# Kernel tuning notes

Measured on AMD Instinct MI355X. Metric: run time of the kernel, lower is better.

The kernel has to match this reference:

```python
import jax, jax.numpy as jnp
from jax import lax
import numpy as np

N_ITERS = 1000
LR = 0.1
EPS = 1e-8


def _log_mag_loss(sos, target_dB):
    """MSE between 20*log10(|sosfreqz(sos)|) and target_dB (matches LogMagTargetFrequencyLoss)."""
    n = target_dB.shape[-1]
    w = jnp.linspace(0.0, np.pi, n)            # [n] freqs in [0, pi]
    z1 = jnp.exp(-1j * w.astype(jnp.complex64))  # e^{-jw}, [n]
    z2 = z1 * z1                               # e^{-2jw}
    b = sos[:, :3].astype(jnp.complex64)       # [16,3] numerator coeffs
    a = sos[:, 3:].astype(jnp.complex64)       # [16,3] denominator coeffs
    # per-section response: (b0 + b1 z^-1 + b2 z^-2) / (a0 + a1 z^-1 + a2 z^-2), [16,n]
    B = b[:, 0:1] + b[:, 1:2] * z1[None, :] + b[:, 2:3] * z2[None, :]
    A = a[:, 0:1] + a[:, 1:2] * z1[None, :] + a[:, 2:3] * z2[None, :]
    H = jnp.prod(B / A, axis=0)                # cascade of sections, [n]
    mag = jnp.sqrt(jnp.real(H) ** 2 + jnp.imag(H) ** 2)
    input_dB = 20.0 * jnp.log10(mag + EPS)
    return jnp.mean((input_dB - target_dB) ** 2)


def setup_inputs() -> dict:
    key = jax.random.key(0)
    k1, k2 = jax.random.split(key)
    sos_init = jax.random.uniform(k1, (16, 6), dtype=jnp.float32)  # torch.rand(16,6)
    target_dB = jax.random.normal(k2, (512,), dtype=jnp.float32) * 6.0  # dB-scale target curve
    return {"sos_init": sos_init, "target_dB": target_dB}


def reference(sos_init, target_dB):
    grad_fn = jax.grad(_log_mag_loss)

    def step(sos, _):
        g = grad_fn(sos, target_dB)
        return sos - LR * g, None  # plain SGD step (no momentum)

    sos_final, _ = lax.scan(step, sos_init, None, length=N_ITERS)
    return sos_final
```

## Files before the change

kernel.cpp:

```cpp
#include <hip/hip_runtime.h>
#include <math.h>

#define TPB 1024

typedef float v2f __attribute__((ext_vector_type(2)));
typedef float v4f __attribute__((ext_vector_type(4)));

static __device__ __forceinline__ v2f mk2(float x, float y) {
    v2f r; r.x = x; r.y = y; return r;
}
static __device__ __forceinline__ v2f fma2(v2f a, v2f b, v2f c) {
    return __builtin_elementwise_fma(a, b, c);
}
static __device__ __forceinline__ v2f rcp2(v2f x) {
    v2f r;
    r.x = __builtin_amdgcn_rcpf(x.x);
    r.y = __builtin_amdgcn_rcpf(x.y);
    return r;
}

static __device__ __forceinline__ void quad_allsum2(float& a, float& b) {
    asm("s_nop 1\n\t"
        "v_add_f32 %0, %0, %0 quad_perm:[1,0,3,2] row_mask:0xf bank_mask:0xf bound_ctrl:0\n\t"
        "v_add_f32 %1, %1, %1 quad_perm:[1,0,3,2] row_mask:0xf bank_mask:0xf bound_ctrl:0\n\t"
        "s_nop 0\n\t"
        "v_add_f32 %0, %0, %0 quad_perm:[2,3,0,1] row_mask:0xf bank_mask:0xf bound_ctrl:0\n\t"
        "v_add_f32 %1, %1, %1 quad_perm:[2,3,0,1] row_mask:0xf bank_mask:0xf bound_ctrl:0"
        : "+v"(a), "+v"(b));
}

__device__ __forceinline__ void red6_s8(float i0, float i1, float i2,
                                        float i3, float i4, float i5,
                                        float& o0, float& o1, float& o2,
                                        float& o3, float& o4, float& o5) {
    asm("s_nop 1\n\t"
        "v_add_f32 %0, %6, %6  row_shr:8 row_mask:0xf bank_mask:0xf bound_ctrl:0\n\t"
        "v_add_f32 %3, %9, %9  row_shr:8 row_mask:0xf bank_mask:0xf bound_ctrl:0\n\t"
        "v_add_f32 %1, %7, %7  row_shr:8 row_mask:0xf bank_mask:0xf bound_ctrl:0\n\t"
        "v_add_f32 %4, %10, %10 row_shr:8 row_mask:0xf bank_mask:0xf bound_ctrl:0\n\t"
        "v_add_f32 %2, %8, %8  row_shr:8 row_mask:0xf bank_mask:0xf bound_ctrl:0\n\t"
        "v_add_f32 %5, %11, %11 row_shr:8 row_mask:0xf bank_mask:0xf bound_ctrl:0"
        : "=&v"(o0), "=&v"(o1), "=&v"(o2), "=&v"(o3), "=&v"(o4), "=&v"(o5)
        : "v"(i0), "v"(i1), "v"(i2), "v"(i3), "v"(i4), "v"(i5));
}

__device__ __forceinline__ void red4_g32(float& a, float& b,
                                         float& c, float& d) {
    asm("s_nop 1\n\t"
        "v_add_f32 %0, %0, %0 row_shr:1 row_mask:0xf bank_mask:0xf bound_ctrl:0\n\t"
        "v_add_f32 %1, %1, %1 row_shr:1 row_mask:0xf bank_mask:0xf bound_ctrl:0\n\t"
        "v_add_f32 %2, %2, %2 row_shr:1 row_mask:0xf bank_mask:0xf bound_ctrl:0\n\t"
        "v_add_f32 %3, %3, %3 row_shr:1 row_mask:0xf bank_mask:0xf bound_ctrl:0\n\t"
        "v_add_f32 %0, %0, %0 row_shr:2 row_mask:0xf bank_mask:0xf bound_ctrl:0\n\t"
        "v_add_f32 %1, %1, %1 row_shr:2 row_mask:0xf bank_mask:0xf bound_ctrl:0\n\t"
        "v_add_f32 %2, %2, %2 row_shr:2 row_mask:0xf bank_mask:0xf bound_ctrl:0\n\t"
        "v_add_f32 %3, %3, %3 row_shr:2 row_mask:0xf bank_mask:0xf bound_ctrl:0\n\t"
        "v_add_f32 %0, %0, %0 row_shr:4 row_mask:0xf bank_mask:0xf bound_ctrl:0\n\t"
        "v_add_f32 %1, %1, %1 row_shr:4 row_mask:0xf bank_mask:0xf bound_ctrl:0\n\t"
        "v_add_f32 %2, %2, %2 row_shr:4 row_mask:0xf bank_mask:0xf bound_ctrl:0\n\t"
        "v_add_f32 %3, %3, %3 row_shr:4 row_mask:0xf bank_mask:0xf bound_ctrl:0\n\t"
        "v_add_f32 %0, %0, %0 row_shr:8 row_mask:0xf bank_mask:0xf bound_ctrl:0\n\t"
        "v_add_f32 %1, %1, %1 row_shr:8 row_mask:0xf bank_mask:0xf bound_ctrl:0\n\t"
        "v_add_f32 %2, %2, %2 row_shr:8 row_mask:0xf bank_mask:0xf bound_ctrl:0\n\t"
        "v_add_f32 %3, %3, %3 row_shr:8 row_mask:0xf bank_mask:0xf bound_ctrl:0\n\t"
        "v_add_f32 %0, %0, %0 row_bcast:15 row_mask:0xa bank_mask:0xf\n\t"
        "v_add_f32 %1, %1, %1 row_bcast:15 row_mask:0xa bank_mask:0xf\n\t"
        "v_add_f32 %2, %2, %2 row_bcast:15 row_mask:0xa bank_mask:0xf\n\t"
        "v_add_f32 %3, %3, %3 row_bcast:15 row_mask:0xa bank_mask:0xf"
        : "+v"(a), "+v"(b), "+v"(c), "+v"(d));
}

__device__ __forceinline__ int cmap(int k) {
    return (k < 3) ? 2 * k : 2 * k - 5;
}

#define GPAD 132

__global__
__attribute__((amdgpu_flat_work_group_size(TPB, TPB), amdgpu_waves_per_eu(4, 4)))
void sgd_filter(const float* __restrict__ sos_in,
                const float* __restrict__ target,
                float* __restrict__ out) {
    __shared__ __align__(16) float sos[96];
    __shared__ __align__(16) float gpart[128][GPAD];

    const int tid = threadIdx.x;
    const int qd  = tid >> 2;
    const int pos = tid & 3;
    const float* secbase = &sos[pos * 24];

    if (tid < 96) sos[(tid / 6) * 6 + cmap(tid % 6)] = sos_in[tid];

    const int c    = tid >> 5;
    const int j    = tid & 31;
    const int slot = c >> 1;
    const int h    = c & 1;
    const int us   = 4 * (slot & 3) + (slot >> 2);
    const bool owner = ((tid & 31) == 31);
    const float* urp = &gpart[j][4 * c];
    float k0 = 0.f, k1 = 0.f, k2 = 0.f, k3 = 0.f;
    if (owner) {
        if (h == 0) {
            k0 = sos_in[6 * us + 0]; k1 = sos_in[6 * us + 3];
            k2 = sos_in[6 * us + 1]; k3 = sos_in[6 * us + 4];
        } else {
            k0 = sos_in[6 * us + 2]; k1 = sos_in[6 * us + 5];
        }
    }

    const double step = 3.14159265358979323846 / 511.0;
    const float w0 = (float)((double)(2 * qd) * step);
    const float w1 = (float)((double)(2 * qd + 1) * step);
    const float c10 = cosf(w0), s10 = -sinf(w0);
    const float c20 = c10 * c10 - s10 * s10, s20 = 2.0f * c10 * s10;
    const float c11 = cosf(w1), s11 = -sinf(w1);
    const float c21 = c11 * c11 - s11 * s11, s21 = 2.0f * c11 * s11;
    const float2 tg = *(const float2*)&target[2 * qd];
    const float KC = 40.0f / (512.0f * 2.302585092994046f);

    const v2f c1v0 = mk2(c10, c10), s1v0 = mk2(s10, s10);
    const v2f c2v0 = mk2(c20, c20), s2v0 = mk2(s20, s20);
    const v2f c1v1 = mk2(c11, c11), s1v1 = mk2(s11, s11);
    const v2f c2v1 = mk2(c21, c21), s2v1 = mk2(s21, s21);

    __syncthreads();

    v2f RA0, RA1, RA2, RA3, IA0, IA1, IA2, IA3;
    v2f RB0, RB1, RB2, RB3, IB0, IB1, IB2, IB3;
    v2f NA0, NA1, NA2, NA3, NB0, NB1, NB2, NB3;

#define SEC_EVAL(sl, BA0, BA1, BA2)                                         \
    {                                                                       \
        const v2f ba0 = BA0, ba1 = BA1, ba2 = BA2;                          \
        RA##sl = fma2(ba2, c2v0, fma2(ba1, c1v0, ba0));                     \
        IA##sl = fma2(ba2, s2v0, ba1 * s1v0);                               \
        NA##sl = fma2(RA##sl, RA##sl, IA##sl * IA##sl);                     \
        RB##sl = fma2(ba2, c2v1, fma2(ba1, c1v1, ba0));                     \
        IB##sl = fma2(ba2, s2v1, ba1 * s1v1);                               \
        NB##sl = fma2(RB##sl, RB##sl, IB##sl * IB##sl);                     \
    }

#define SEC_BWD(sl)                                                         \
    {                                                                       \
        const v2f PA = WA##sl * RA##sl;                                     \
        const v2f QA = WA##sl * IA##sl;                                     \
        const v2f PB = WB##sl * RB##sl;                                     \
        const v2f QB = WB##sl * IB##sl;                                     \
        const v2f P  = PA + PB;                                             \
        const v2f G1 = fma2(c1v1, PB, fma2(s1v1, QB,                        \
                       fma2(c1v0, PA, s1v0 * QA)));                         \
        const v2f G2 = fma2(c2v1, PB, fma2(s2v1, QB,                        \
                       fma2(c2v0, PA, s2v0 * QA)));                         \
        float g0, g1, g2, g3, g4, g5;                                       \
        red6_s8(P.x, G1.x, G2.x, P.y, G1.y, G2.y,                           \
                g0, g1, g2, g3, g4, g5);                                    \
        if ((tid & 15) >= 8) {                                              \
            float* p = &gpart[((tid >> 4) << 1) | ((tid >> 2) & 1)]         \
                             [8 * (4 * (sl) + pos)];                        \
            *(float4*)p       = make_float4(g0, g3, g1, g4);                \
            *(float2*)(p + 4) = make_float2(g2, g5);                        \
        }                                                                   \
    }

    for (int it = 0; it < 1000; ++it) {
        const float4 q0 = *(const float4*)(secbase + 0);
        const float4 q1 = *(const float4*)(secbase + 4);
        const float4 q2 = *(const float4*)(secbase + 8);
        const float4 q3 = *(const float4*)(secbase + 12);
        const float4 q4 = *(const float4*)(secbase + 16);
        const float4 q5 = *(const float4*)(secbase + 20);
        SEC_EVAL(0, mk2(q0.x, q0.y), mk2(q0.z, q0.w), mk2(q1.x, q1.y))
        SEC_EVAL(1, mk2(q1.z, q1.w), mk2(q2.x, q2.y), mk2(q2.z, q2.w))
        SEC_EVAL(2, mk2(q3.x, q3.y), mk2(q3.z, q3.w), mk2(q4.x, q4.y))
        SEC_EVAL(3, mk2(q4.z, q4.w), mk2(q5.x, q5.y), mk2(q5.z, q5.w))

        const v2f tA01 = NA0 * NA1, tA23 = NA2 * NA3;
        const v2f mA   = tA01 * tA23;
        const v2f iA   = rcp2(mA);
        const v2f tB01 = NB0 * NB1, tB23 = NB2 * NB3;
        const v2f mB   = tB01 * tB23;
        const v2f iB   = rcp2(mB);
        float L0 = __builtin_amdgcn_logf(mA.x * iA.y);
        float L1 = __builtin_amdgcn_logf(mB.x * iB.y);

        quad_allsum2(L0, L1);

        const float mag0   = __builtin_amdgcn_exp2f(0.5f * L0);
        const float magpe0 = mag0 + 1e-8f;
        const float indB0  = 6.020599913279624f * __builtin_amdgcn_logf(magpe0);
        const float K0 = KC * (indB0 - tg.x) * mag0 * __builtin_amdgcn_rcpf(magpe0);
        const float mag1   = __builtin_amdgcn_exp2f(0.5f * L1);
        const float magpe1 = mag1 + 1e-8f;
        const float indB1  = 6.020599913279624f * __builtin_amdgcn_logf(magpe1);
        const float K1 = KC * (indB1 - tg.y) * mag1 * __builtin_amdgcn_rcpf(magpe1);
        const v2f KK0 = mk2(K0, -K0);
        const v2f KK1 = mk2(K1, -K1);

        const v2f jA   = KK0 * iA;
        const v2f jA01 = jA * tA23, jA23 = jA * tA01;
        const v2f WA0 = jA01 * NA1, WA1 = jA01 * NA0;
        const v2f WA2 = jA23 * NA3, WA3 = jA23 * NA2;
        const v2f jB   = KK1 * iB;
        const v2f jB01 = jB * tB23, jB23 = jB * tB01;
        const v2f WB0 = jB01 * NB1, WB1 = jB01 * NB0;
        const v2f WB2 = jB23 * NB3, WB3 = jB23 * NB2;

        SEC_BWD(0) SEC_BWD(1) SEC_BWD(2) SEC_BWD(3)
        __syncthreads();

        {
            const v4f p0 = *(const v4f*)urp;
            const v4f p1 = *(const v4f*)(urp + 32 * GPAD);
            const v4f p2 = *(const v4f*)(urp + 64 * GPAD);
            const v4f p3 = *(const v4f*)(urp + 96 * GPAD);
            const v4f s = (p0 + p1) + (p2 + p3);
            float t0 = s.x, t1 = s.y, t2 = s.z, t3 = s.w;
            red4_g32(t0, t1, t2, t3);
            if (owner) {
                k0 = fmaf(-0.1f, t0, k0);
                k1 = fmaf(-0.1f, t1, k1);
                k2 = fmaf(-0.1f, t2, k2);
                k3 = fmaf(-0.1f, t3, k3);
                if (h == 0) {
                    *(float2*)&sos[6 * us]     = make_float2(k0, k1);
                    *(float2*)&sos[6 * us + 2] = make_float2(k2, k3);
                } else {
                    *(float2*)&sos[6 * us + 4] = make_float2(k0, k1);
                }
            }
        }
        __syncthreads();
    }

    if (owner) {
        if (h == 0) {
            out[6 * us + 0] = k0; out[6 * us + 3] = k1;
            out[6 * us + 1] = k2; out[6 * us + 4] = k3;
        } else {
            out[6 * us + 2] = k0; out[6 * us + 5] = k1;
        }
    }
}

extern "C" void kernel_launch(void* const* d_in, const int* in_sizes, int n_in,
                              void* d_out, int out_size, void* d_ws, size_t ws_size,
                              hipStream_t stream) {
    const float* sos_in = (const float*)d_in[0];
    const float* target = (const float*)d_in[1];
    float* outp = (float*)d_out;
    hipLaunchKernelGGL(sgd_filter, dim3(1), dim3(TPB), 0, stream, sos_in, target, outp);
}
```

Measured before the change: 1.960 ms.

## Pack gradient partials densely, replace log-sum with product-sqrt, fold dB constants

The gradient partial buffer is repacked so each writer lane stores 24 contiguous floats with six float4 stores, and GPAD shrinks to 100. Only 24 waves, with 4 coefficients each, now perform the reduction and the float4 sos update, replacing the earlier half-slot layout with its branching. The per-quad log-sum followed by exp2 is replaced with a DPP product reduction followed by sqrt, and the dB scaling constants are folded into one fma. The product form could overflow or underflow in float32 where the log-sum form would not.

```diff
diff --git a/kernel.cpp b/kernel.cpp
--- a/kernel.cpp
+++ b/kernel.cpp
@@ -19,13 +19,13 @@
     return r;
 }
 
-static __device__ __forceinline__ void quad_allsum2(float& a, float& b) {
+static __device__ __forceinline__ void quad_allprod2(float& a, float& b) {
     asm("s_nop 1\n\t"
-        "v_add_f32 %0, %0, %0 quad_perm:[1,0,3,2] row_mask:0xf bank_mask:0xf bound_ctrl:0\n\t"
-        "v_add_f32 %1, %1, %1 quad_perm:[1,0,3,2] row_mask:0xf bank_mask:0xf bound_ctrl:0\n\t"
+        "v_mul_f32 %0, %0, %0 quad_perm:[1,0,3,2] row_mask:0xf bank_mask:0xf bound_ctrl:0\n\t"
+        "v_mul_f32 %1, %1, %1 quad_perm:[1,0,3,2] row_mask:0xf bank_mask:0xf bound_ctrl:0\n\t"
         "s_nop 0\n\t"
-        "v_add_f32 %0, %0, %0 quad_perm:[2,3,0,1] row_mask:0xf bank_mask:0xf bound_ctrl:0\n\t"
-        "v_add_f32 %1, %1, %1 quad_perm:[2,3,0,1] row_mask:0xf bank_mask:0xf bound_ctrl:0"
+        "v_mul_f32 %0, %0, %0 quad_perm:[2,3,0,1] row_mask:0xf bank_mask:0xf bound_ctrl:0\n\t"
+        "v_mul_f32 %1, %1, %1 quad_perm:[2,3,0,1] row_mask:0xf bank_mask:0xf bound_ctrl:0"
         : "+v"(a), "+v"(b));
 }
 
@@ -73,8 +73,12 @@
 __device__ __forceinline__ int cmap(int k) {
     return (k < 3) ? 2 * k : 2 * k - 5;
 }
-
-#define GPAD 132
+__device__ __forceinline__ int oidx(int cid) {
+    const int s = cid / 6, p = cid % 6;
+    return 6 * s + ((p & 1) ? 3 + (p >> 1) : (p >> 1));
+}
+
+#define GPAD 100
 
 __global__
 __attribute__((amdgpu_flat_work_group_size(TPB, TPB), amdgpu_waves_per_eu(4, 4)))
@@ -88,24 +92,21 @@
     const int qd  = tid >> 2;
     const int pos = tid & 3;
     const float* secbase = &sos[pos * 24];
+    const int brow = ((tid >> 4) << 1) | ((tid >> 2) & 1);
 
     if (tid < 96) sos[(tid / 6) * 6 + cmap(tid % 6)] = sos_in[tid];
 
     const int c    = tid >> 5;
     const int j    = tid & 31;
-    const int slot = c >> 1;
-    const int h    = c & 1;
-    const int us   = 4 * (slot & 3) + (slot >> 2);
-    const bool owner = ((tid & 31) == 31);
-    const float* urp = &gpart[j][4 * c];
+    const bool upd   = (c < 24);
+    const bool owner = upd && (j == 31);
+    const float* urp = &gpart[j][4 * (c & 31)];
+    const int oi0 = oidx(4 * c + 0), oi1 = oidx(4 * c + 1);
+    const int oi2 = oidx(4 * c + 2), oi3 = oidx(4 * c + 3);
     float k0 = 0.f, k1 = 0.f, k2 = 0.f, k3 = 0.f;
     if (owner) {
-        if (h == 0) {
-            k0 = sos_in[6 * us + 0]; k1 = sos_in[6 * us + 3];
-            k2 = sos_in[6 * us + 1]; k3 = sos_in[6 * us + 4];
-        } else {
-            k0 = sos_in[6 * us + 2]; k1 = sos_in[6 * us + 5];
-        }
+        k0 = sos_in[oi0]; k1 = sos_in[oi1];
+        k2 = sos_in[oi2]; k3 = sos_in[oi3];
     }
 
     const double step = 3.14159265358979323846 / 511.0;
@@ -117,6 +118,9 @@
     const float c21 = c11 * c11 - s11 * s11, s21 = 2.0f * c11 * s11;
     const float2 tg = *(const float2*)&target[2 * qd];
     const float KC = 40.0f / (512.0f * 2.302585092994046f);
+    const float A2   = KC * 6.020599913279624f;
+    const float nKt0 = -KC * tg.x;
+    const float nKt1 = -KC * tg.y;
 
     const v2f c1v0 = mk2(c10, c10), s1v0 = mk2(s10, s10);
     const v2f c2v0 = mk2(c20, c20), s2v0 = mk2(s20, s20);
@@ -140,7 +144,8 @@
         NB##sl = fma2(RB##sl, RB##sl, IB##sl * IB##sl);                     \
     }
 
-#define SEC_BWD(sl)                                                         \
+#define SEC_BWD(sl, g)                                                      \
+    float g##0, g##1, g##2, g##3, g##4, g##5;                               \
     {                                                                       \
         const v2f PA = WA##sl * RA##sl;                                     \
         const v2f QA = WA##sl * IA##sl;                                     \
@@ -151,15 +156,8 @@
                        fma2(c1v0, PA, s1v0 * QA)));                         \
         const v2f G2 = fma2(c2v1, PB, fma2(s2v1, QB,                        \
                        fma2(c2v0, PA, s2v0 * QA)));                         \
-        float g0, g1, g2, g3, g4, g5;                                       \
         red6_s8(P.x, G1.x, G2.x, P.y, G1.y, G2.y,                           \
-                g0, g1, g2, g3, g4, g5);                                    \
-        if ((tid & 15) >= 8) {                                              \
-            float* p = &gpart[((tid >> 4) << 1) | ((tid >> 2) & 1)]         \
-                             [8 * (4 * (sl) + pos)];                        \
-            *(float4*)p       = make_float4(g0, g3, g1, g4);                \
-            *(float2*)(p + 4) = make_float2(g2, g5);                        \
-        }                                                                   \
+                g##0, g##1, g##2, g##3, g##4, g##5);                        \
     }
 
     for (int it = 0; it < 1000; ++it) {
@@ -180,19 +178,19 @@
         const v2f tB01 = NB0 * NB1, tB23 = NB2 * NB3;
         const v2f mB   = tB01 * tB23;
         const v2f iB   = rcp2(mB);
-        float L0 = __builtin_amdgcn_logf(mA.x * iA.y);
-        float L1 = __builtin_amdgcn_logf(mB.x * iB.y);
-
-        quad_allsum2(L0, L1);
-
-        const float mag0   = __builtin_amdgcn_exp2f(0.5f * L0);
+        float r0 = mA.x * iA.y;
+        float r1 = mB.x * iB.y;
+
+        quad_allprod2(r0, r1);
+
+        const float mag0   = __builtin_amdgcn_sqrtf(r0);
         const float magpe0 = mag0 + 1e-8f;
-        const float indB0  = 6.020599913279624f * __builtin_amdgcn_logf(magpe0);
-        const float K0 = KC * (indB0 - tg.x) * mag0 * __builtin_amdgcn_rcpf(magpe0);
-        const float mag1   = __builtin_amdgcn_exp2f(0.5f * L1);
+        const float t0c    = fmaf(A2, __builtin_amdgcn_logf(magpe0), nKt0);
+        const float K0     = t0c * mag0 * __builtin_amdgcn_rcpf(magpe0);
+        const float mag1   = __builtin_amdgcn_sqrtf(r1);
         const float magpe1 = mag1 + 1e-8f;
-        const float indB1  = 6.020599913279624f * __builtin_amdgcn_logf(magpe1);
-        const float K1 = KC * (indB1 - tg.y) * mag1 * __builtin_amdgcn_rcpf(magpe1);
+        const float t1c    = fmaf(A2, __builtin_amdgcn_logf(magpe1), nKt1);
+        const float K1     = t1c * mag1 * __builtin_amdgcn_rcpf(magpe1);
         const v2f KK0 = mk2(K0, -K0);
         const v2f KK1 = mk2(K1, -K1);
 
@@ -205,10 +203,19 @@
         const v2f WB0 = jB01 * NB1, WB1 = jB01 * NB0;
         const v2f WB2 = jB23 * NB3, WB3 = jB23 * NB2;
 
-        SEC_BWD(0) SEC_BWD(1) SEC_BWD(2) SEC_BWD(3)
+        SEC_BWD(0, ga) SEC_BWD(1, gb) SEC_BWD(2, gc) SEC_BWD(3, gd)
+        if ((tid & 15) >= 8) {
+            float4* p = (float4*)&gpart[brow][24 * pos];
+            p[0] = make_float4(ga0, ga3, ga1, ga4);
+            p[1] = make_float4(ga2, ga5, gb0, gb3);
+            p[2] = make_float4(gb1, gb4, gb2, gb5);
+            p[3] = make_float4(gc0, gc3, gc1, gc4);
+            p[4] = make_float4(gc2, gc5, gd0, gd3);
+            p[5] = make_float4(gd1, gd4, gd2, gd5);
+        }
         __syncthreads();
 
-        {
+        if (upd) {
             const v4f p0 = *(const v4f*)urp;
             const v4f p1 = *(const v4f*)(urp + 32 * GPAD);
             const v4f p2 = *(const v4f*)(urp + 64 * GPAD);
@@ -221,24 +228,15 @@
                 k1 = fmaf(-0.1f, t1, k1);
                 k2 = fmaf(-0.1f, t2, k2);
                 k3 = fmaf(-0.1f, t3, k3);
-                if (h == 0) {
-                    *(float2*)&sos[6 * us]     = make_float2(k0, k1);
-                    *(float2*)&sos[6 * us + 2] = make_float2(k2, k3);
-                } else {
-                    *(float2*)&sos[6 * us + 4] = make_float2(k0, k1);
-                }
+                *(float4*)&sos[4 * c] = make_float4(k0, k1, k2, k3);
             }
         }
         __syncthreads();
     }
 
     if (owner) {
-        if (h == 0) {
-            out[6 * us + 0] = k0; out[6 * us + 3] = k1;
-            out[6 * us + 1] = k2; out[6 * us + 4] = k3;
-        } else {
-            out[6 * us + 2] = k0; out[6 * us + 5] = k1;
-        }
+        out[oi0] = k0; out[oi1] = k1;
+        out[oi2] = k2; out[oi3] = k3;
     }
 }
 
```

Result: faster. 1.856 ms, median of 2 (-5.3%).
